# Performance work log

Hardware: AMD Instinct MI355X
Metric: run time of the kernel (lower is better)

## Reference

```python
import jax, jax.numpy as jnp
import numpy as np

NUM_NODES = 100000
EMBED_DIM = 64
HIDDEN_DIM = 64
HEADS = 4
NEG_SLOPE = 0.2


def setup_inputs() -> dict:
    key = jax.random.key(0)
    ks = jax.random.split(key, 10)
    E = 1000000
    edge_index = jax.random.randint(ks[0], (2, E), 0, NUM_NODES, dtype=jnp.int64)
    out1 = HIDDEN_DIM // HEADS  # 16
    s = 1.0 / np.sqrt(EMBED_DIM)
    emb = jax.random.normal(ks[1], (NUM_NODES, EMBED_DIM), jnp.float32) * s
    # Layer 1: GATConv(64 -> 16, heads=4, concat=True)
    W1 = jax.random.normal(ks[2], (EMBED_DIM, HEADS * out1), jnp.float32) * s
    a_src1 = jax.random.normal(ks[3], (HEADS, out1), jnp.float32) * 0.1
    a_dst1 = jax.random.normal(ks[4], (HEADS, out1), jnp.float32) * 0.1
    b1 = jnp.zeros((HEADS * out1,), jnp.float32)
    # Layer 2: GATConv(64 -> 64, heads=1, concat=False)
    W2 = jax.random.normal(ks[5], (HIDDEN_DIM, HIDDEN_DIM), jnp.float32) * s
    a_src2 = jax.random.normal(ks[6], (1, HIDDEN_DIM), jnp.float32) * 0.1
    a_dst2 = jax.random.normal(ks[7], (1, HIDDEN_DIM), jnp.float32) * 0.1
    b2 = jnp.zeros((HIDDEN_DIM,), jnp.float32)
    return {"edge_index": edge_index, "emb": emb,
            "W1": W1, "a_src1": a_src1, "a_dst1": a_dst1, "b1": b1,
            "W2": W2, "a_src2": a_src2, "a_dst2": a_dst2, "b2": b2}


def _gat_conv(x, src, dst, num_nodes, W, a_s, a_d, heads, out_ch):
    # x: [N, F_in]; messages flow src -> dst, softmax over incoming edges of dst.
    h = (x @ W).reshape(-1, heads, out_ch)            # [N, H, C]
    alpha_s = (h * a_s[None]).sum(-1)                 # [N, H]
    alpha_d = (h * a_d[None]).sum(-1)                 # [N, H]
    e = alpha_s[src] + alpha_d[dst]                   # [E, H]
    e = jnp.where(e > 0, e, NEG_SLOPE * e)            # LeakyReLU(0.2)
    m = jax.ops.segment_max(e, dst, num_segments=num_nodes)   # [N, H]
    w = jnp.exp(e - m[dst])                           # [E, H]
    denom = jax.ops.segment_sum(w, dst, num_segments=num_nodes)
    alpha = w / (denom[dst] + 1e-16)                  # [E, H]
    out = jax.ops.segment_sum(alpha[:, :, None] * h[src], dst,
                              num_segments=num_nodes)  # [N, H, C]
    return out


def _forward(edge_index, emb, W1, a_src1, a_dst1, b1, W2, a_src2, a_dst2, b2):
    N = emb.shape[0]
    loops = jnp.arange(N, dtype=edge_index.dtype)
    src = jnp.concatenate([edge_index[0], loops])  # PyG add_self_loops=True
    dst = jnp.concatenate([edge_index[1], loops])
    # Layer 1: heads=4, concat
    x = _gat_conv(emb, src, dst, N, W1, a_src1, a_dst1, HEADS, HIDDEN_DIM // HEADS)
    x = x.reshape(N, -1) + b1                      # concat heads -> [N, 64]
    x = jax.nn.elu(x)
    # Layer 2: heads=1, concat=False (mean over the single head)
    x = _gat_conv(x, src, dst, N, W2, a_src2, a_dst2, 1, HIDDEN_DIM)
    x = x[:, 0, :] + b2                            # [N, 64]
    # F.normalize(p=2, dim=1) with eps=1e-12
    norm = jnp.maximum(jnp.linalg.norm(x, axis=1, keepdims=True), 1e-12)
    return x / norm


def reference(edge_index, emb, W1, a_src1, a_dst1, b1, W2, a_src2, a_dst2, b2):
    return _forward(edge_index, emb, W1, a_src1, a_dst1, b1, W2, a_src2, a_dst2, b2)
```

## Files before the change

### kernel.cpp

```cpp
#include <hip/hip_runtime.h>
#include <hip/hip_fp16.h>
#include <math.h>


constexpr int FDIM = 64;
constexpr int BSHIFT = 9;
constexpr int BMASK = (1 << BSHIFT) - 1;
constexpr int EDGE_TILE = 4096;

using f16 = _Float16;
typedef f16 f16x8 __attribute__((ext_vector_type(8)));
typedef f16 f16x4 __attribute__((ext_vector_type(4)));
typedef float f32x4 __attribute__((ext_vector_type(4)));


__global__ void zero_kernel(int* __restrict__ p, int n) {
  int i = blockIdx.x * blockDim.x + threadIdx.x;
  if (i < n) p[i] = 0;
}


__global__ __launch_bounds__(256) void tile_hist_kernel(
    const int* __restrict__ ei, int E, int Etot, int NB,
    int* __restrict__ gbhist) {
  __shared__ int hist[512];
  int t = threadIdx.x;
  for (int b = t; b < NB; b += 256) hist[b] = 0;
  __syncthreads();
  int i0 = blockIdx.x * EDGE_TILE;
  int iend = min(i0 + EDGE_TILE, Etot);
  for (int i = i0 + t; i < iend; i += 256) {
    int dst = (i < E) ? ei[E + i] : (i - E);
    atomicAdd(&hist[dst >> BSHIFT], 1);
  }
  __syncthreads();
  for (int b = t; b < NB; b += 256)
    if (hist[b]) atomicAdd(&gbhist[b], hist[b]);
}

__global__ __launch_bounds__(256) void bscan_kernel(
    const int* __restrict__ gbhist, int NB, int Etot,
    int* __restrict__ boff, int* __restrict__ bcur) {
  int t = threadIdx.x;
  int v = (t < NB) ? gbhist[t] : 0;
  int lane = t & 63, w = t >> 6;
  int x = v;
#pragma unroll
  for (int off = 1; off < 64; off <<= 1) {
    int u = __shfl_up(x, off, 64);
    if (lane >= off) x += u;
  }
  __shared__ int wsum[4];
  if (lane == 63) wsum[w] = x;
  __syncthreads();
  int add = 0;
#pragma unroll
  for (int k = 0; k < 4; ++k) add += (k < w) ? wsum[k] : 0;
  int incl = x + add;
  if (t < NB) {
    boff[t] = incl - v;
    bcur[t] = incl - v;
  }
  if (t == 0) boff[NB] = Etot;
}

__global__ __launch_bounds__(256) void tile_scatter_kernel(
    const int* __restrict__ ei, int E, int Etot, int NB,
    int* __restrict__ bcur, unsigned* __restrict__ bpacked) {
  __shared__ int hist[512];
  __shared__ int cur[512];
  int t = threadIdx.x;
  for (int b = t; b < NB; b += 256) hist[b] = 0;
  __syncthreads();
  int i0 = blockIdx.x * EDGE_TILE;
  int iend = min(i0 + EDGE_TILE, Etot);
  for (int i = i0 + t; i < iend; i += 256) {
    int dst = (i < E) ? ei[E + i] : (i - E);
    atomicAdd(&hist[dst >> BSHIFT], 1);
  }
  __syncthreads();
  for (int b = t; b < NB; b += 256)
    cur[b] = hist[b] ? atomicAdd(&bcur[b], hist[b]) : 0;
  __syncthreads();
  for (int i = i0 + t; i < iend; i += 256) {
    int src, dst;
    if (i < E) { src = ei[i]; dst = ei[E + i]; }
    else       { src = i - E; dst = i - E; }
    int pos = atomicAdd(&cur[dst >> BSHIFT], 1);
    bpacked[pos] = ((unsigned)src << BSHIFT) | (unsigned)(dst & BMASK);
  }
}

__global__ __launch_bounds__(256) void bucket_csr_kernel(
    const unsigned* __restrict__ bpacked, const int* __restrict__ boff,
    int N, int NB, int Etot,
    int* __restrict__ row_start, int* __restrict__ esrc) {
  __shared__ int hist[512];
  __shared__ int excl[512];
  __shared__ int cur[512];
  int b = blockIdx.x;
  int t = threadIdx.x;
  int base = boff[b];
  int end = boff[b + 1];
  hist[t] = 0;
  hist[256 + t] = 0;
  __syncthreads();
  for (int i = base + t; i < end; i += 256)
    atomicAdd(&hist[bpacked[i] & (unsigned)BMASK], 1);
  __syncthreads();
  int h0 = hist[2 * t], h1 = hist[2 * t + 1];
  int s = h0 + h1;
  int lane = t & 63, w = t >> 6;
  int x = s;
#pragma unroll
  for (int off = 1; off < 64; off <<= 1) {
    int u = __shfl_up(x, off, 64);
    if (lane >= off) x += u;
  }
  __shared__ int wsum[4];
  if (lane == 63) wsum[w] = x;
  __syncthreads();
  int add = 0;
#pragma unroll
  for (int k = 0; k < 4; ++k) add += (k < w) ? wsum[k] : 0;
  int e0 = x + add - s;
  excl[2 * t] = e0;
  excl[2 * t + 1] = e0 + h0;
  cur[2 * t] = e0;
  cur[2 * t + 1] = e0 + h0;
  __syncthreads();
  int node0 = b << BSHIFT;
#pragma unroll
  for (int k = 0; k < 2; ++k) {
    int slot = k * 256 + t;
    int node = node0 + slot;
    if (node < N) row_start[node] = base + excl[slot];
  }
  if (b == NB - 1 && t == 0) row_start[N] = Etot;
  for (int i = base + t; i < end; i += 256) {
    unsigned p = bpacked[i];
    int pos = base + atomicAdd(&cur[p & (unsigned)BMASK], 1);
    esrc[pos] = (int)(p >> BSHIFT);
  }
}


template <int HEADS, typename IN>
__global__ __launch_bounds__(256) void mfma_gemm_kernel(
    const IN* __restrict__ X, const float* __restrict__ W,
    const float* __restrict__ a_s, const float* __restrict__ a_d, int N,
    __half* __restrict__ H, float* __restrict__ AS, float* __restrict__ AD) {
  __shared__ f16 Xs[64 * 72];
  __shared__ f16 Wt[64 * 72];
  int t = threadIdx.x;
  int row0 = blockIdx.x * 64;

#pragma unroll
  for (int i = 0; i < 16; ++i) {
    int idx = i * 256 + t;
    int k = idx >> 6, c = idx & 63;
    Wt[c * 72 + k] = (f16)W[idx];
  }
  if constexpr (sizeof(IN) == 4) {
#pragma unroll
    for (int i = 0; i < 4; ++i) {
      int idx = (i * 256 + t) * 4;
      int r = idx >> 6, k = idx & 63;
      int rg = min(row0 + r, N - 1);
      float4 f = *reinterpret_cast<const float4*>(
          reinterpret_cast<const float*>(X) + (size_t)rg * 64 + k);
      f16x4 v = {(f16)f.x, (f16)f.y, (f16)f.z, (f16)f.w};
      *reinterpret_cast<f16x4*>(&Xs[r * 72 + k]) = v;
    }
  } else {
#pragma unroll
    for (int i = 0; i < 2; ++i) {
      int idx = (i * 256 + t) * 8;
      int r = idx >> 6, k = idx & 63;
      int rg = min(row0 + r, N - 1);
      f16x8 v = *reinterpret_cast<const f16x8*>(
          reinterpret_cast<const f16*>(X) + (size_t)rg * 64 + k);
      *reinterpret_cast<f16x8*>(&Xs[r * 72 + k]) = v;
    }
  }
  __syncthreads();

  int lane = t & 63, wid = t >> 6;
  int m0 = wid * 16;
  int li = lane & 15, lk = lane >> 4;
  int ko = lk * 8;

  f16x8 a_lo = *reinterpret_cast<const f16x8*>(&Xs[(m0 + li) * 72 + ko]);
  f16x8 a_hi = *reinterpret_cast<const f16x8*>(&Xs[(m0 + li) * 72 + 32 + ko]);

  f32x4 acc[4];
  float asc[4], adc[4];
#pragma unroll
  for (int q = 0; q < 4; ++q) {
    acc[q] = (f32x4){0.f, 0.f, 0.f, 0.f};
    asc[q] = a_s[q * 16 + li];
    adc[q] = a_d[q * 16 + li];
  }
#pragma unroll
  for (int q = 0; q < 4; ++q) {
    int c0 = q * 16 + li;
    f16x8 b_lo = *reinterpret_cast<const f16x8*>(&Wt[c0 * 72 + ko]);
    f16x8 b_hi = *reinterpret_cast<const f16x8*>(&Wt[c0 * 72 + 32 + ko]);
    acc[q] = __builtin_amdgcn_mfma_f32_16x16x32_f16(a_lo, b_lo, acc[q], 0, 0, 0);
    acc[q] = __builtin_amdgcn_mfma_f32_16x16x32_f16(a_hi, b_hi, acc[q], 0, 0, 0);
  }

  int rbase = row0 + m0 + lk * 4;
#pragma unroll
  for (int r = 0; r < 4; ++r) {
    int grow = rbase + r;
    if (grow < N) {
#pragma unroll
      for (int q = 0; q < 4; ++q)
        H[(size_t)grow * 64 + q * 16 + li] = __float2half((float)acc[q][r]);
    }
  }

  if constexpr (HEADS == 4) {
    float ps[4][4], pd[4][4];
#pragma unroll
    for (int q = 0; q < 4; ++q)
#pragma unroll
      for (int r = 0; r < 4; ++r) {
        ps[q][r] = (float)acc[q][r] * asc[q];
        pd[q][r] = (float)acc[q][r] * adc[q];
      }
#pragma unroll
    for (int off = 1; off < 16; off <<= 1)
#pragma unroll
      for (int q = 0; q < 4; ++q)
#pragma unroll
        for (int r = 0; r < 4; ++r) {
          ps[q][r] += __shfl_xor(ps[q][r], off, 64);
          pd[q][r] += __shfl_xor(pd[q][r], off, 64);
        }
    if (li == 0) {
#pragma unroll
      for (int r = 0; r < 4; ++r) {
        int grow = rbase + r;
        if (grow < N) {
#pragma unroll
          for (int q = 0; q < 4; ++q) {
            AS[(size_t)grow * 4 + q] = ps[q][r];
            AD[(size_t)grow * 4 + q] = pd[q][r];
          }
        }
      }
    }
  } else {
    float ps[4], pd[4];
#pragma unroll
    for (int r = 0; r < 4; ++r) {
      ps[r] = 0.f; pd[r] = 0.f;
#pragma unroll
      for (int q = 0; q < 4; ++q) {
        ps[r] = fmaf((float)acc[q][r], asc[q], ps[r]);
        pd[r] = fmaf((float)acc[q][r], adc[q], pd[r]);
      }
    }
#pragma unroll
    for (int off = 1; off < 16; off <<= 1)
#pragma unroll
      for (int r = 0; r < 4; ++r) {
        ps[r] += __shfl_xor(ps[r], off, 64);
        pd[r] += __shfl_xor(pd[r], off, 64);
      }
    if (li == 0) {
#pragma unroll
      for (int r = 0; r < 4; ++r) {
        int grow = rbase + r;
        if (grow < N) { AS[grow] = ps[r]; AD[grow] = pd[r]; }
      }
    }
  }
}


template <int HEADS, bool FINAL, typename OUTT>
__global__ __launch_bounds__(256) void aggregate_kernel(
    const int* __restrict__ row_start, const int* __restrict__ esrc,
    const __half* __restrict__ H, const float* __restrict__ AS,
    const float* __restrict__ AD, const float* __restrict__ bias, int N,
    OUTT* __restrict__ OUT) {
  int t = threadIdx.x;
  int wid = t >> 6;
  int half = (t >> 5) & 1;
  int ll = t & 31;
  int n = blockIdx.x * 8 + wid * 2 + half;

  constexpr int G = 64 / HEADS;
  int head = (2 * ll) / G;

  int rs = 0, re = 0;
  float ad = 0.f;
  if (n < N) {
    rs = row_start[n];
    re = row_start[n + 1];
    ad = AD[(size_t)n * HEADS + head];
  }
  int deg = re - rs;
  int degO = __shfl_xor(deg, 32, 64);
  int degmax = max(deg, degO);

  const __half2* H2 = reinterpret_cast<const __half2*>(H);

  float d[4] = {0.f, 0.f, 0.f, 0.f};
  float ax[4] = {0.f, 0.f, 0.f, 0.f};
  float ay[4] = {0.f, 0.f, 0.f, 0.f};

  for (int i = 0; i < degmax; i += 4) {
    int sv[4];
#pragma unroll
    for (int k = 0; k < 4; ++k) {
      int o = min(i + k, deg - 1);
      o = max(o, 0);
      sv[k] = esrc[rs + o];
    }
    float ev[4];
    __half2 hv[4];
#pragma unroll
    for (int k = 0; k < 4; ++k) {
      ev[k] = AS[(unsigned)sv[k] * HEADS + (unsigned)head];
      hv[k] = H2[(unsigned)sv[k] * 32u + (unsigned)ll];
    }
#pragma unroll
    for (int k = 0; k < 4; ++k) {
      float e = ev[k] + ad;
      e = fmaxf(e, 0.2f * e);
      float wg = (i + k < deg) ? __expf(e) : 0.f;
      float2 hf = __half22float2(hv[k]);
      d[k] += wg;
      ax[k] = fmaf(wg, hf.x, ax[k]);
      ay[k] = fmaf(wg, hf.y, ay[k]);
    }
  }

  if (n >= N) return;

  float denom = (d[0] + d[1]) + (d[2] + d[3]);
  float axs = (ax[0] + ax[1]) + (ax[2] + ax[3]);
  float ays = (ay[0] + ay[1]) + (ay[2] + ay[3]);

  float2 b2 = reinterpret_cast<const float2*>(bias)[ll];
  float inv = 1.f / (denom + 1e-16f);
  float vx = axs * inv + b2.x;
  float vy = ays * inv + b2.y;
  if constexpr (FINAL) {
    float ss = vx * vx + vy * vy;
#pragma unroll
    for (int off = 1; off < 32; off <<= 1) ss += __shfl_xor(ss, off, 32);
    float rn = 1.f / fmaxf(sqrtf(ss), 1e-12f);
    float2* OUT2 = reinterpret_cast<float2*>(OUT);
    OUT2[(size_t)n * 32 + ll] = make_float2(vx * rn, vy * rn);
  } else {
    vx = vx > 0.f ? vx : expm1f(vx);
    vy = vy > 0.f ? vy : expm1f(vy);
    __half2* OUT2 = reinterpret_cast<__half2*>(OUT);
    OUT2[(size_t)n * 32 + ll] = __floats2half2_rn(vx, vy);
  }
}


extern "C" void kernel_launch(void* const* d_in, const int* in_sizes, int n_in,
                              void* d_out, int out_size, void* d_ws,
                              size_t ws_size, hipStream_t stream) {
  const int* ei = (const int*)d_in[0];
  const float* emb = (const float*)d_in[1];
  const float* W1 = (const float*)d_in[2];
  const float* as1 = (const float*)d_in[3];
  const float* ad1 = (const float*)d_in[4];
  const float* b1 = (const float*)d_in[5];
  const float* W2 = (const float*)d_in[6];
  const float* as2 = (const float*)d_in[7];
  const float* ad2 = (const float*)d_in[8];
  const float* b2 = (const float*)d_in[9];
  float* out = (float*)d_out;

  int E = in_sizes[0] / 2;
  int N = in_sizes[1] / FDIM;
  int Etot = E + N;
  int NB = (N + BMASK) >> BSHIFT;
  int nTiles = (Etot + EDGE_TILE - 1) / EDGE_TILE;

  char* ws = (char*)d_ws;
  size_t off = 0;
  auto alloc = [&](size_t bytes) -> void* {
    void* p = ws + off;
    off += (bytes + 255) & ~(size_t)255;
    return p;
  };
  int* gbhist = (int*)alloc((size_t)NB * sizeof(int));
  int* boff = (int*)alloc((size_t)(NB + 1) * sizeof(int));
  int* bcur = (int*)alloc((size_t)NB * sizeof(int));
  unsigned* bpacked = (unsigned*)alloc((size_t)Etot * sizeof(unsigned));
  int* row_start = (int*)alloc((size_t)(N + 1) * sizeof(int));
  int* esrc = (int*)alloc((size_t)Etot * sizeof(int));
  __half* hbuf = (__half*)alloc((size_t)N * FDIM * sizeof(__half));
  __half* xbuf = (__half*)alloc((size_t)N * FDIM * sizeof(__half));
  float* AS = (float*)alloc((size_t)N * 4 * sizeof(float));
  float* AD = (float*)alloc((size_t)N * 4 * sizeof(float));

  zero_kernel<<<(NB + 255) / 256, 256, 0, stream>>>(gbhist, NB);
  tile_hist_kernel<<<nTiles, 256, 0, stream>>>(ei, E, Etot, NB, gbhist);
  bscan_kernel<<<1, 256, 0, stream>>>(gbhist, NB, Etot, boff, bcur);
  tile_scatter_kernel<<<nTiles, 256, 0, stream>>>(ei, E, Etot, NB, bcur, bpacked);
  bucket_csr_kernel<<<NB, 256, 0, stream>>>(bpacked, boff, N, NB, Etot,
                                            row_start, esrc);

  int gm = (N + 63) / 64;
  int ga = (N + 7) / 8;
  mfma_gemm_kernel<4, float><<<gm, 256, 0, stream>>>(emb, W1, as1, ad1, N, hbuf, AS, AD);
  aggregate_kernel<4, false, __half><<<ga, 256, 0, stream>>>(row_start, esrc, hbuf, AS, AD, b1, N, xbuf);
  mfma_gemm_kernel<1, __half><<<gm, 256, 0, stream>>>(xbuf, W2, as2, ad2, N, hbuf, AS, AD);
  aggregate_kernel<1, true, float><<<ga, 256, 0, stream>>>(row_start, esrc, hbuf, AS, AD, b2, N, out);
}
```

Baseline: 155.0 us.

## Precompute per-edge attention weights in separate kernel and widen aggregate lanes

Adds an edge_weight_kernel that computes exp(LeakyReLU(AS[src]+AD[dst])) per edge and stores it as fp16, using a new edst array written during CSR construction. The aggregate kernel now reads these precomputed weights instead of gathering AS per edge and running exp. It also changes the lane mapping so each lane handles 4 channels and two edges are processed in parallel per half-wave, followed by a shuffle reduction. The aim is to take the random AS gather and the redundant per-lane exp out of the hot loop. The cost is extra global traffic (writing and reading Etot*HEADS fp16 weights plus edst), two extra launches, and fp16 rounding of the weights.

```diff
diff --git a/kernel.cpp b/kernel.cpp
--- a/kernel.cpp
+++ b/kernel.cpp
@@ -94,7 +94,8 @@
 __global__ __launch_bounds__(256) void bucket_csr_kernel(
     const unsigned* __restrict__ bpacked, const int* __restrict__ boff,
     int N, int NB, int Etot,
-    int* __restrict__ row_start, int* __restrict__ esrc) {
+    int* __restrict__ row_start, int* __restrict__ esrc,
+    int* __restrict__ edst) {
   __shared__ int hist[512];
   __shared__ int excl[512];
   __shared__ int cur[512];
@@ -139,8 +140,10 @@
   if (b == NB - 1 && t == 0) row_start[N] = Etot;
   for (int i = base + t; i < end; i += 256) {
     unsigned p = bpacked[i];
-    int pos = base + atomicAdd(&cur[p & (unsigned)BMASK], 1);
+    int slot = (int)(p & (unsigned)BMASK);
+    int pos = base + atomicAdd(&cur[slot], 1);
     esrc[pos] = (int)(p >> BSHIFT);
+    edst[pos] = node0 + slot;
   }
 }
 
@@ -281,87 +284,110 @@
 }
 
 
+template <int HEADS>
+__global__ __launch_bounds__(256) void edge_weight_kernel(
+    const int* __restrict__ esrc, const int* __restrict__ edst,
+    const float* __restrict__ AS, const float* __restrict__ AD, int Etot,
+    __half* __restrict__ Wg) {
+  int i = blockIdx.x * 256 + threadIdx.x;
+  if (i >= Etot) return;
+  int s = esrc[i], dd = edst[i];
+  if constexpr (HEADS == 4) {
+    float4 a4 = *reinterpret_cast<const float4*>(&AS[(size_t)s * 4]);
+    float4 d4 = *reinterpret_cast<const float4*>(&AD[(size_t)dd * 4]);
+    float e0 = a4.x + d4.x, e1 = a4.y + d4.y;
+    float e2 = a4.z + d4.z, e3 = a4.w + d4.w;
+    e0 = fmaxf(e0, 0.2f * e0); e1 = fmaxf(e1, 0.2f * e1);
+    e2 = fmaxf(e2, 0.2f * e2); e3 = fmaxf(e3, 0.2f * e3);
+    __half2* W2 = reinterpret_cast<__half2*>(Wg);
+    W2[2 * i]     = __floats2half2_rn(__expf(e0), __expf(e1));
+    W2[2 * i + 1] = __floats2half2_rn(__expf(e2), __expf(e3));
+  } else {
+    float e = AS[s] + AD[dd];
+    e = fmaxf(e, 0.2f * e);
+    Wg[i] = __float2half(__expf(e));
+  }
+}
+
+
 template <int HEADS, bool FINAL, typename OUTT>
 __global__ __launch_bounds__(256) void aggregate_kernel(
     const int* __restrict__ row_start, const int* __restrict__ esrc,
-    const __half* __restrict__ H, const float* __restrict__ AS,
-    const float* __restrict__ AD, const float* __restrict__ bias, int N,
-    OUTT* __restrict__ OUT) {
+    const __half* __restrict__ Wg, const __half* __restrict__ H,
+    const float* __restrict__ bias, int N, OUTT* __restrict__ OUT) {
   int t = threadIdx.x;
   int wid = t >> 6;
   int half = (t >> 5) & 1;
   int ll = t & 31;
+  int c = ll & 15;
+  int eo = ll >> 4;
   int n = blockIdx.x * 8 + wid * 2 + half;
 
-  constexpr int G = 64 / HEADS;
-  int head = (2 * ll) / G;
+  int head = (HEADS == 4) ? (c >> 2) : 0;
 
   int rs = 0, re = 0;
-  float ad = 0.f;
   if (n < N) {
     rs = row_start[n];
     re = row_start[n + 1];
-    ad = AD[(size_t)n * HEADS + head];
   }
   int deg = re - rs;
   int degO = __shfl_xor(deg, 32, 64);
   int degmax = max(deg, degO);
 
-  const __half2* H2 = reinterpret_cast<const __half2*>(H);
-
-  float d[4] = {0.f, 0.f, 0.f, 0.f};
-  float ax[4] = {0.f, 0.f, 0.f, 0.f};
-  float ay[4] = {0.f, 0.f, 0.f, 0.f};
-
+  const f16* Hp = reinterpret_cast<const f16*>(H);
+
+  float d = 0.f, a0 = 0.f, a1 = 0.f, a2 = 0.f, a3 = 0.f;
   for (int i = 0; i < degmax; i += 4) {
-    int sv[4];
-#pragma unroll
-    for (int k = 0; k < 4; ++k) {
-      int o = min(i + k, deg - 1);
-      o = max(o, 0);
-      sv[k] = esrc[rs + o];
-    }
-    float ev[4];
-    __half2 hv[4];
-#pragma unroll
-    for (int k = 0; k < 4; ++k) {
-      ev[k] = AS[(unsigned)sv[k] * HEADS + (unsigned)head];
-      hv[k] = H2[(unsigned)sv[k] * 32u + (unsigned)ll];
-    }
-#pragma unroll
-    for (int k = 0; k < 4; ++k) {
-      float e = ev[k] + ad;
-      e = fmaxf(e, 0.2f * e);
-      float wg = (i + k < deg) ? __expf(e) : 0.f;
-      float2 hf = __half22float2(hv[k]);
-      d[k] += wg;
-      ax[k] = fmaf(wg, hf.x, ax[k]);
-      ay[k] = fmaf(wg, hf.y, ay[k]);
-    }
-  }
+#pragma unroll
+    for (int k = 0; k < 2; ++k) {
+      int o = i + 2 * k + eo;
+      int oc = min(o, deg - 1);
+      oc = max(oc, 0);
+      int s = esrc[rs + oc];
+      float w = (float)Wg[(unsigned)(rs + oc) * HEADS + (unsigned)head];
+      w = (o < deg) ? w : 0.f;
+      f16x4 h4 = *reinterpret_cast<const f16x4*>(&Hp[(size_t)s * 64 + c * 4]);
+      d += w;
+      a0 = fmaf(w, (float)h4[0], a0);
+      a1 = fmaf(w, (float)h4[1], a1);
+      a2 = fmaf(w, (float)h4[2], a2);
+      a3 = fmaf(w, (float)h4[3], a3);
+    }
+  }
+
+  d  += __shfl_xor(d, 16, 64);
+  a0 += __shfl_xor(a0, 16, 64);
+  a1 += __shfl_xor(a1, 16, 64);
+  a2 += __shfl_xor(a2, 16, 64);
+  a3 += __shfl_xor(a3, 16, 64);
 
   if (n >= N) return;
 
-  float denom = (d[0] + d[1]) + (d[2] + d[3]);
-  float axs = (ax[0] + ax[1]) + (ax[2] + ax[3]);
-  float ays = (ay[0] + ay[1]) + (ay[2] + ay[3]);
-
-  float2 b2 = reinterpret_cast<const float2*>(bias)[ll];
-  float inv = 1.f / (denom + 1e-16f);
-  float vx = axs * inv + b2.x;
-  float vy = ays * inv + b2.y;
+  float inv = 1.f / (d + 1e-16f);
+  float4 b4 = reinterpret_cast<const float4*>(bias)[c];
+  float v0 = a0 * inv + b4.x;
+  float v1 = a1 * inv + b4.y;
+  float v2 = a2 * inv + b4.z;
+  float v3 = a3 * inv + b4.w;
+
   if constexpr (FINAL) {
-    float ss = vx * vx + vy * vy;
-#pragma unroll
-    for (int off = 1; off < 32; off <<= 1) ss += __shfl_xor(ss, off, 32);
+    float ss = v0 * v0 + v1 * v1 + v2 * v2 + v3 * v3;
+#pragma unroll
+    for (int off = 1; off < 16; off <<= 1) ss += __shfl_xor(ss, off, 64);
     float rn = 1.f / fmaxf(sqrtf(ss), 1e-12f);
-    float2* OUT2 = reinterpret_cast<float2*>(OUT);
-    OUT2[(size_t)n * 32 + ll] = make_float2(vx * rn, vy * rn);
+    if (eo == 0) {
+      float4* O4 = reinterpret_cast<float4*>(OUT);
+      O4[(size_t)n * 16 + c] = make_float4(v0 * rn, v1 * rn, v2 * rn, v3 * rn);
+    }
   } else {
-    vx = vx > 0.f ? vx : expm1f(vx);
-    vy = vy > 0.f ? vy : expm1f(vy);
-    __half2* OUT2 = reinterpret_cast<__half2*>(OUT);
-    OUT2[(size_t)n * 32 + ll] = __floats2half2_rn(vx, vy);
+    v0 = v0 > 0.f ? v0 : expm1f(v0);
+    v1 = v1 > 0.f ? v1 : expm1f(v1);
+    v2 = v2 > 0.f ? v2 : expm1f(v2);
+    v3 = v3 > 0.f ? v3 : expm1f(v3);
+    if (eo == 0) {
+      f16x4 o = {(f16)v0, (f16)v1, (f16)v2, (f16)v3};
+      reinterpret_cast<f16x4*>(OUT)[(size_t)n * 16 + c] = o;
+    }
   }
 }
 
@@ -400,6 +426,8 @@
   unsigned* bpacked = (unsigned*)alloc((size_t)Etot * sizeof(unsigned));
   int* row_start = (int*)alloc((size_t)(N + 1) * sizeof(int));
   int* esrc = (int*)alloc((size_t)Etot * sizeof(int));
+  int* edst = (int*)alloc((size_t)Etot * sizeof(int));
+  __half* Wg = (__half*)alloc((size_t)Etot * 4 * sizeof(__half));
   __half* hbuf = (__half*)alloc((size_t)N * FDIM * sizeof(__half));
   __half* xbuf = (__half*)alloc((size_t)N * FDIM * sizeof(__half));
   float* AS = (float*)alloc((size_t)N * 4 * sizeof(float));
@@ -410,12 +438,16 @@
   bscan_kernel<<<1, 256, 0, stream>>>(gbhist, NB, Etot, boff, bcur);
   tile_scatter_kernel<<<nTiles, 256, 0, stream>>>(ei, E, Etot, NB, bcur, bpacked);
   bucket_csr_kernel<<<NB, 256, 0, stream>>>(bpacked, boff, N, NB, Etot,
-                                            row_start, esrc);
+                                            row_start, esrc, edst);
 
   int gm = (N + 63) / 64;
   int ga = (N + 7) / 8;
+  int ge = (Etot + 255) / 256;
+
   mfma_gemm_kernel<4, float><<<gm, 256, 0, stream>>>(emb, W1, as1, ad1, N, hbuf, AS, AD);
-  aggregate_kernel<4, false, __half><<<ga, 256, 0, stream>>>(row_start, esrc, hbuf, AS, AD, b1, N, xbuf);
+  edge_weight_kernel<4><<<ge, 256, 0, stream>>>(esrc, edst, AS, AD, Etot, Wg);
+  aggregate_kernel<4, false, __half><<<ga, 256, 0, stream>>>(row_start, esrc, Wg, hbuf, b1, N, xbuf);
   mfma_gemm_kernel<1, __half><<<gm, 256, 0, stream>>>(xbuf, W2, as2, ad2, N, hbuf, AS, AD);
-  aggregate_kernel<1, true, float><<<ga, 256, 0, stream>>>(row_start, esrc, hbuf, AS, AD, b2, N, out);
-}
+  edge_weight_kernel<1><<<ge, 256, 0, stream>>>(esrc, edst, AS, AD, Etot, Wg);
+  aggregate_kernel<1, true, float><<<ga, 256, 0, stream>>>(row_start, esrc, Wg, hbuf, b2, N, out);
+}
```

Result: slower. 168.1 us (+8.5%).
